# Kernel optimization log

Hardware: AMD Instinct MI355X
Metric: run time of the kernel (lower is better)

The kernel has to match this reference:

```python
import jax, jax.numpy as jnp
import numpy as np

B, IN, OUT = 512, 1023, 512
CLIP = 2.0
LN_EPS = 1e-5


def setup_inputs() -> dict:
    key = jax.random.key(0)
    ks = jax.random.split(key, 10)
    x = jax.random.normal(ks[0], (B, IN), dtype=jnp.float32)
    hebb = jax.random.normal(ks[1], (B, IN + 1, OUT), dtype=jnp.float32)
    weight = 0.001 * jax.random.normal(ks[2], (IN + 1, OUT), dtype=jnp.float32)
    alpha = 0.001 * jax.random.normal(ks[3], (IN + 1, OUT), dtype=jnp.float32)
    ln_gamma = jnp.ones((OUT,), dtype=jnp.float32)
    ln_beta = jnp.zeros((OUT,), dtype=jnp.float32)
    # modulator: Linear(OUT, 1)
    mod_w = jax.random.uniform(ks[4], (1, OUT), dtype=jnp.float32,
                               minval=-1.0, maxval=1.0) / np.sqrt(OUT)
    mod_b = jax.random.uniform(ks[5], (1,), dtype=jnp.float32,
                               minval=-1.0, maxval=1.0) / np.sqrt(OUT)
    # modfanout: Linear(1, OUT)
    fan_w = jax.random.uniform(ks[6], (OUT, 1), dtype=jnp.float32,
                               minval=-1.0, maxval=1.0)
    fan_b = jax.random.uniform(ks[7], (OUT,), dtype=jnp.float32,
                               minval=-1.0, maxval=1.0)
    return {"x": x, "hebb": hebb, "weight": weight, "alpha": alpha,
            "ln_gamma": ln_gamma, "ln_beta": ln_beta,
            "mod_w": mod_w, "mod_b": mod_b, "fan_w": fan_w, "fan_b": fan_b}


def reference(x, hebb, weight, alpha, ln_gamma, ln_beta, mod_w, mod_b, fan_w, fan_b):
    # pad bias column of ones: [B, IN+1]
    xp = jnp.concatenate([x, jnp.ones((x.shape[0], 1), dtype=x.dtype)], axis=-1)
    # per-sample effective weights: [B, IN+1, OUT]
    w_eff = weight[None] + alpha[None] * hebb
    y_pre = jnp.einsum('bi,bio->bo', xp, w_eff)  # [B, OUT]
    # LayerNorm over last dim
    mu = jnp.mean(y_pre, axis=-1, keepdims=True)
    var = jnp.mean(jnp.square(y_pre - mu), axis=-1, keepdims=True)
    y = jnp.tanh(ln_gamma * (y_pre - mu) * jax.lax.rsqrt(var + LN_EPS) + ln_beta)
    # modulator scalar per sample: [B, 1]
    m = jnp.tanh(y @ mod_w.T + mod_b)
    # fanout eta: [B, 1, OUT]
    eta = m[:, :, None] * fan_w[:, 0][None, None, :] + fan_b[None, None, :]
    # outer-product Hebbian update: [B, IN+1, OUT]
    delta = eta * (xp[:, :, None] * y[:, None, :])
    hebb_new = jnp.clip(hebb + delta, -CLIP, CLIP)
    return (y, m, hebb_new)
```

## Files before the change

### kernel.cpp

```cpp
#include <hip/hip_runtime.h>
#include <cstddef>

#define B_    512
#define IN_   1023
#define INP1  1024
#define OUT_  512
#define OUT4  128
#define CLIPV 2.0f
#define LNEPS 1e-5f

__device__ __forceinline__ float2 block_reduce2(float a, float b, float2* lds) {
    #pragma unroll
    for (int off = 32; off; off >>= 1) {
        a += __shfl_down(a, off, 64);
        b += __shfl_down(b, off, 64);
    }
    const int lane = threadIdx.x & 63;
    const int wid  = threadIdx.x >> 6;
    const int nw   = blockDim.x >> 6;
    if (lane == 0) lds[wid] = make_float2(a, b);
    __syncthreads();
    if (wid == 0) {
        float2 v = (lane < nw) ? lds[lane] : make_float2(0.f, 0.f);
        a = v.x; b = v.y;
        #pragma unroll
        for (int off = 8; off; off >>= 1) {
            a += __shfl_down(a, off, 64);
            b += __shfl_down(b, off, 64);
        }
        if (lane == 0) lds[0] = make_float2(a, b);
    }
    __syncthreads();
    float2 r = lds[0];
    __syncthreads();
    return r;
}

__global__ __launch_bounds__(1024) void k1_ypre_ln_mod(
    const float* __restrict__ x, const float* __restrict__ hebb,
    const float* __restrict__ weight, const float* __restrict__ alpha,
    const float* __restrict__ ln_g, const float* __restrict__ ln_b,
    const float* __restrict__ mod_w, const float* __restrict__ mod_b,
    float* __restrict__ y_out, float* __restrict__ m_out)
{
    const int b     = blockIdx.x;
    const int tid   = threadIdx.x;
    const int o4    = tid & 127;
    const int chunk = tid >> 7;

    const float4* __restrict__ h4 = (const float4*)hebb + (size_t)b * (INP1 * OUT4);
    const float4* __restrict__ w4 = (const float4*)weight;
    const float4* __restrict__ a4 = (const float4*)alpha;
    const float*  __restrict__ xr = x + (size_t)b * IN_;

    float4 acc = make_float4(0.f, 0.f, 0.f, 0.f);
    const int i0 = chunk * 128;
    #pragma unroll 4
    for (int k = 0; k < 128; ++k) {
        const int i = i0 + k;
        const float xv = (i < IN_) ? xr[i] : 1.0f;
        const float4 h = h4[(size_t)i * OUT4 + o4];
        const float4 w = w4[i * OUT4 + o4];
        const float4 a = a4[i * OUT4 + o4];
        acc.x = fmaf(xv, fmaf(a.x, h.x, w.x), acc.x);
        acc.y = fmaf(xv, fmaf(a.y, h.y, w.y), acc.y);
        acc.z = fmaf(xv, fmaf(a.z, h.z, w.z), acc.z);
        acc.w = fmaf(xv, fmaf(a.w, h.w, w.w), acc.w);
    }

    __shared__ float  part[8][OUT_];
    __shared__ float2 rbuf[16];
    ((float4*)part[chunk])[o4] = acc;
    __syncthreads();

    const int o = tid;
    float ypre = 0.f;
    if (tid < OUT_) {
        #pragma unroll
        for (int c = 0; c < 8; ++c) ypre += part[c][o];
    }

    const float va = (tid < OUT_) ? ypre : 0.f;
    float2 ss = block_reduce2(va, va * va, rbuf);
    const float mu   = ss.x * (1.0f / OUT_);
    const float var  = ss.y * (1.0f / OUT_) - mu * mu;
    const float rstd = rsqrtf(var + LNEPS);

    float yv = 0.f;
    if (tid < OUT_) {
        yv = tanhf(fmaf(ln_g[o], (ypre - mu) * rstd, ln_b[o]));
        y_out[(size_t)b * OUT_ + o] = yv;
    }

    float2 ms = block_reduce2((tid < OUT_) ? yv * mod_w[o] : 0.f, 0.f, rbuf);
    if (tid == 0) m_out[b] = tanhf(ms.x + mod_b[0]);
}

__global__ __launch_bounds__(256) void k2_hebb_update(
    const float* __restrict__ x, const float* __restrict__ hebb,
    const float* __restrict__ y, const float* __restrict__ m,
    const float* __restrict__ fan_w, const float* __restrict__ fan_b,
    float* __restrict__ hebb_out)
{
    const size_t total4 = (size_t)B_ * INP1 * OUT4;
    const size_t stride = (size_t)gridDim.x * blockDim.x;
    for (size_t idx = (size_t)blockIdx.x * blockDim.x + threadIdx.x;
         idx < total4; idx += stride) {
        const int o4 = (int)(idx & (OUT4 - 1));
        const int i  = (int)((idx >> 7) & (INP1 - 1));
        const int b  = (int)(idx >> 17);

        const float xv = (i < IN_) ? x[(size_t)b * IN_ + i] : 1.0f;
        const float mb = m[b];
        const float4 h  = ((const float4*)hebb)[idx];
        const float4 yv = ((const float4*)y)[(size_t)b * OUT4 + o4];
        const float4 fw = ((const float4*)fan_w)[o4];
        const float4 fb = ((const float4*)fan_b)[o4];

        float4 r;
        r.x = fminf(fmaxf(fmaf(fmaf(mb, fw.x, fb.x) * xv, yv.x, h.x), -CLIPV), CLIPV);
        r.y = fminf(fmaxf(fmaf(fmaf(mb, fw.y, fb.y) * xv, yv.y, h.y), -CLIPV), CLIPV);
        r.z = fminf(fmaxf(fmaf(fmaf(mb, fw.z, fb.z) * xv, yv.z, h.z), -CLIPV), CLIPV);
        r.w = fminf(fmaxf(fmaf(fmaf(mb, fw.w, fb.w) * xv, yv.w, h.w), -CLIPV), CLIPV);
        ((float4*)hebb_out)[idx] = r;
    }
}

extern "C" void kernel_launch(void* const* d_in, const int* in_sizes, int n_in,
                              void* d_out, int out_size, void* d_ws, size_t ws_size,
                              hipStream_t stream) {
    const float* x      = (const float*)d_in[0];
    const float* hebb   = (const float*)d_in[1];
    const float* weight = (const float*)d_in[2];
    const float* alpha  = (const float*)d_in[3];
    const float* ln_g   = (const float*)d_in[4];
    const float* ln_b   = (const float*)d_in[5];
    const float* mod_w  = (const float*)d_in[6];
    const float* mod_b  = (const float*)d_in[7];
    const float* fan_w  = (const float*)d_in[8];
    const float* fan_b  = (const float*)d_in[9];

    float* out      = (float*)d_out;
    float* y_out    = out;
    float* m_out    = out + (size_t)B_ * OUT_;
    float* hebb_out = m_out + B_;

    k1_ypre_ln_mod<<<B_, 1024, 0, stream>>>(x, hebb, weight, alpha,
                                            ln_g, ln_b, mod_w, mod_b,
                                            y_out, m_out);

    k2_hebb_update<<<8192, 256, 0, stream>>>(x, hebb, y_out, m_out,
                                             fan_w, fan_b, hebb_out);
}
```

Before: 714.0 us.

## Split row reduction into slab partials and reverse-order slab update for L2 reuse

The first pass now splits each sample's 1024 rows into four 256-row slabs handled by separate 256-thread blocks. Partial sums go to workspace, and a small kernel finishes LayerNorm and the modulator. The update kernel walks the same slabs in reverse block order, so the most recently read hebb slabs may still sit in cache. It also precomputes eta*y per column, stages x in LDS, and uses nontemporal stores. This trades an extra launch and a workspace round trip for better occupancy, and it falls back to using hebb_out as scratch when the workspace is too small.

```diff
diff --git a/kernel.cpp b/kernel.cpp
--- a/kernel.cpp
+++ b/kernel.cpp
@@ -1,13 +1,17 @@
 #include <hip/hip_runtime.h>
 #include <cstddef>
 
-#define B_    512
-#define IN_   1023
-#define INP1  1024
-#define OUT_  512
-#define OUT4  128
-#define CLIPV 2.0f
-#define LNEPS 1e-5f
+#define B_       512
+#define IN_      1023
+#define INP1     1024
+#define OUT_     512
+#define OUT4     128
+#define CLIPV    2.0f
+#define LNEPS    1e-5f
+#define SLABS    4
+#define SLABROWS 256
+
+typedef float fx4 __attribute__((ext_vector_type(4)));
 
 __device__ __forceinline__ float2 block_reduce2(float a, float b, float2* lds) {
     #pragma unroll
@@ -36,93 +40,129 @@
     return r;
 }
 
-__global__ __launch_bounds__(1024) void k1_ypre_ln_mod(
+__global__ __launch_bounds__(256) void k1a_partial(
     const float* __restrict__ x, const float* __restrict__ hebb,
     const float* __restrict__ weight, const float* __restrict__ alpha,
-    const float* __restrict__ ln_g, const float* __restrict__ ln_b,
-    const float* __restrict__ mod_w, const float* __restrict__ mod_b,
-    float* __restrict__ y_out, float* __restrict__ m_out)
+    float* __restrict__ ws_part)
 {
-    const int b     = blockIdx.x;
-    const int tid   = threadIdx.x;
-    const int o4    = tid & 127;
-    const int chunk = tid >> 7;
+    const int bs   = blockIdx.x;
+    const int b    = bs >> 2;
+    const int s    = bs & 3;
+    const int tid  = threadIdx.x;
+    const int o4   = tid & 127;
+    const int half = tid >> 7;
 
-    const float4* __restrict__ h4 = (const float4*)hebb + (size_t)b * (INP1 * OUT4);
-    const float4* __restrict__ w4 = (const float4*)weight;
-    const float4* __restrict__ a4 = (const float4*)alpha;
-    const float*  __restrict__ xr = x + (size_t)b * IN_;
+    __shared__ float  xs[SLABROWS];
+    __shared__ float4 part[2][OUT4];
+
+    {
+        const int i = s * SLABROWS + tid;
+        xs[tid] = (i < IN_) ? x[(size_t)b * IN_ + i] : 1.0f;
+    }
+    __syncthreads();
+
+    const int i0 = s * SLABROWS + half * 128;
+    const float4* __restrict__ h4 = (const float4*)hebb  + ((size_t)b * INP1 + i0) * OUT4 + o4;
+    const float4* __restrict__ w4 = (const float4*)weight + (size_t)i0 * OUT4 + o4;
+    const float4* __restrict__ a4 = (const float4*)alpha  + (size_t)i0 * OUT4 + o4;
+    const float* __restrict__ xk = xs + half * 128;
 
     float4 acc = make_float4(0.f, 0.f, 0.f, 0.f);
-    const int i0 = chunk * 128;
     #pragma unroll 4
     for (int k = 0; k < 128; ++k) {
-        const int i = i0 + k;
-        const float xv = (i < IN_) ? xr[i] : 1.0f;
-        const float4 h = h4[(size_t)i * OUT4 + o4];
-        const float4 w = w4[i * OUT4 + o4];
-        const float4 a = a4[i * OUT4 + o4];
+        const float  xv = xk[k];
+        const float4 h  = h4[(size_t)k * OUT4];
+        const float4 w  = w4[(size_t)k * OUT4];
+        const float4 a  = a4[(size_t)k * OUT4];
         acc.x = fmaf(xv, fmaf(a.x, h.x, w.x), acc.x);
         acc.y = fmaf(xv, fmaf(a.y, h.y, w.y), acc.y);
         acc.z = fmaf(xv, fmaf(a.z, h.z, w.z), acc.z);
         acc.w = fmaf(xv, fmaf(a.w, h.w, w.w), acc.w);
     }
 
-    __shared__ float  part[8][OUT_];
+    part[half][o4] = acc;
+    __syncthreads();
+    if (half == 0) {
+        float4 p = part[0][o4];
+        const float4 q = part[1][o4];
+        p.x += q.x; p.y += q.y; p.z += q.z; p.w += q.w;
+        ((float4*)ws_part)[(size_t)bs * OUT4 + o4] = p;
+    }
+}
+
+__global__ __launch_bounds__(512) void k1b_ln_mod(
+    const float* __restrict__ ws_part,
+    const float* __restrict__ ln_g, const float* __restrict__ ln_b,
+    const float* __restrict__ mod_w, const float* __restrict__ mod_b,
+    float* __restrict__ y_out, float* __restrict__ m_out)
+{
+    const int b = blockIdx.x;
+    const int o = threadIdx.x;
     __shared__ float2 rbuf[16];
-    ((float4*)part[chunk])[o4] = acc;
-    __syncthreads();
 
-    const int o = tid;
     float ypre = 0.f;
-    if (tid < OUT_) {
-        #pragma unroll
-        for (int c = 0; c < 8; ++c) ypre += part[c][o];
-    }
+    #pragma unroll
+    for (int s = 0; s < SLABS; ++s)
+        ypre += ws_part[((size_t)b * SLABS + s) * OUT_ + o];
 
-    const float va = (tid < OUT_) ? ypre : 0.f;
-    float2 ss = block_reduce2(va, va * va, rbuf);
+    float2 ss = block_reduce2(ypre, ypre * ypre, rbuf);
     const float mu   = ss.x * (1.0f / OUT_);
     const float var  = ss.y * (1.0f / OUT_) - mu * mu;
     const float rstd = rsqrtf(var + LNEPS);
 
-    float yv = 0.f;
-    if (tid < OUT_) {
-        yv = tanhf(fmaf(ln_g[o], (ypre - mu) * rstd, ln_b[o]));
-        y_out[(size_t)b * OUT_ + o] = yv;
-    }
+    const float yv = tanhf(fmaf(ln_g[o], (ypre - mu) * rstd, ln_b[o]));
+    y_out[(size_t)b * OUT_ + o] = yv;
 
-    float2 ms = block_reduce2((tid < OUT_) ? yv * mod_w[o] : 0.f, 0.f, rbuf);
-    if (tid == 0) m_out[b] = tanhf(ms.x + mod_b[0]);
+    float2 ms = block_reduce2(yv * mod_w[o], 0.f, rbuf);
+    if (o == 0) m_out[b] = tanhf(ms.x + mod_b[0]);
 }
 
-__global__ __launch_bounds__(256) void k2_hebb_update(
+__global__ __launch_bounds__(256) void k2_update(
     const float* __restrict__ x, const float* __restrict__ hebb,
     const float* __restrict__ y, const float* __restrict__ m,
     const float* __restrict__ fan_w, const float* __restrict__ fan_b,
     float* __restrict__ hebb_out)
 {
-    const size_t total4 = (size_t)B_ * INP1 * OUT4;
-    const size_t stride = (size_t)gridDim.x * blockDim.x;
-    for (size_t idx = (size_t)blockIdx.x * blockDim.x + threadIdx.x;
-         idx < total4; idx += stride) {
-        const int o4 = (int)(idx & (OUT4 - 1));
-        const int i  = (int)((idx >> 7) & (INP1 - 1));
-        const int b  = (int)(idx >> 17);
+    const int bsr  = (int)gridDim.x - 1 - (int)blockIdx.x;
+    const int b    = bsr >> 2;
+    const int s    = bsr & 3;
+    const int tid  = threadIdx.x;
+    const int o4   = tid & 127;
+    const int half = tid >> 7;
 
-        const float xv = (i < IN_) ? x[(size_t)b * IN_ + i] : 1.0f;
-        const float mb = m[b];
-        const float4 h  = ((const float4*)hebb)[idx];
-        const float4 yv = ((const float4*)y)[(size_t)b * OUT4 + o4];
-        const float4 fw = ((const float4*)fan_w)[o4];
-        const float4 fb = ((const float4*)fan_b)[o4];
+    __shared__ float xs[SLABROWS];
+    {
+        const int i = s * SLABROWS + tid;
+        xs[tid] = (i < IN_) ? x[(size_t)b * IN_ + i] : 1.0f;
+    }
+    __syncthreads();
 
-        float4 r;
-        r.x = fminf(fmaxf(fmaf(fmaf(mb, fw.x, fb.x) * xv, yv.x, h.x), -CLIPV), CLIPV);
-        r.y = fminf(fmaxf(fmaf(fmaf(mb, fw.y, fb.y) * xv, yv.y, h.y), -CLIPV), CLIPV);
-        r.z = fminf(fmaxf(fmaf(fmaf(mb, fw.z, fb.z) * xv, yv.z, h.z), -CLIPV), CLIPV);
-        r.w = fminf(fmaxf(fmaf(fmaf(mb, fw.w, fb.w) * xv, yv.w, h.w), -CLIPV), CLIPV);
-        ((float4*)hebb_out)[idx] = r;
+    const float  mb = m[b];
+    const float4 yv = ((const float4*)y)[(size_t)b * OUT4 + o4];
+    const float4 fw = ((const float4*)fan_w)[o4];
+    const float4 fb = ((const float4*)fan_b)[o4];
+    float4 coef;
+    coef.x = fmaf(mb, fw.x, fb.x) * yv.x;
+    coef.y = fmaf(mb, fw.y, fb.y) * yv.y;
+    coef.z = fmaf(mb, fw.z, fb.z) * yv.z;
+    coef.w = fmaf(mb, fw.w, fb.w) * yv.w;
+
+    const int i0 = s * SLABROWS + half * 128;
+    const size_t base = ((size_t)b * INP1 + i0) * OUT4 + o4;
+    const fx4* __restrict__ h4  = (const fx4*)hebb + base;
+    fx4* __restrict__       ho4 = (fx4*)hebb_out + base;
+    const float* __restrict__ xk = xs + half * 128;
+
+    #pragma unroll 4
+    for (int k = 0; k < 128; ++k) {
+        const float xv = xk[k];
+        const fx4   h  = h4[(size_t)k * OUT4];
+        fx4 r;
+        r.x = fminf(fmaxf(fmaf(coef.x, xv, h.x), -CLIPV), CLIPV);
+        r.y = fminf(fmaxf(fmaf(coef.y, xv, h.y), -CLIPV), CLIPV);
+        r.z = fminf(fmaxf(fmaf(coef.z, xv, h.z), -CLIPV), CLIPV);
+        r.w = fminf(fmaxf(fmaf(coef.w, xv, h.w), -CLIPV), CLIPV);
+        __builtin_nontemporal_store(r, &ho4[(size_t)k * OUT4]);
     }
 }
 
@@ -145,10 +185,13 @@
     float* m_out    = out + (size_t)B_ * OUT_;
     float* hebb_out = m_out + B_;
 
-    k1_ypre_ln_mod<<<B_, 1024, 0, stream>>>(x, hebb, weight, alpha,
-                                            ln_g, ln_b, mod_w, mod_b,
-                                            y_out, m_out);
+    const size_t part_bytes = (size_t)B_ * SLABS * OUT_ * sizeof(float);
+    float* ws_part = (ws_size >= part_bytes) ? (float*)d_ws
+                                             : hebb_out;
 
-    k2_hebb_update<<<8192, 256, 0, stream>>>(x, hebb, y_out, m_out,
-                                             fan_w, fan_b, hebb_out);
+    k1a_partial<<<B_ * SLABS, 256, 0, stream>>>(x, hebb, weight, alpha, ws_part);
+    k1b_ln_mod<<<B_, OUT_, 0, stream>>>(ws_part, ln_g, ln_b, mod_w, mod_b,
+                                        y_out, m_out);
+    k2_update<<<B_ * SLABS, 256, 0, stream>>>(x, hebb, y_out, m_out,
+                                              fan_w, fan_b, hebb_out);
 }
```

Result: faster. 648.8 us (-9.1%).
